# Optimization experiments

Measured on AMD Instinct MI355X. Metric: run time of the kernel, lower is better.

Reference implementation:

```python
import jax, jax.numpy as jnp
import numpy as np

D = 1024
H = 16
HD = D // H
FF = 4096
B, S = 2, 2048


def _ln(x, g, b, eps):
    mu = jnp.mean(x, axis=-1, keepdims=True)
    var = jnp.mean(jnp.square(x - mu), axis=-1, keepdims=True)
    return (x - mu) * jax.lax.rsqrt(var + eps) * g + b


def setup_inputs() -> dict:
    key = jax.random.key(0)
    ks = jax.random.split(key, 12)
    s = 0.02
    return {
        "x": jax.random.normal(ks[0], (B, S, D), jnp.float32),
        "attention_mask": jnp.ones((B, 1, 1, S), jnp.int32),
        "wq": jax.random.normal(ks[1], (D, D), jnp.float32) * s,
        "bq": jnp.zeros((D,), jnp.float32),
        "wk": jax.random.normal(ks[2], (D, D), jnp.float32) * s,
        "bk": jnp.zeros((D,), jnp.float32),
        "wv": jax.random.normal(ks[3], (D, D), jnp.float32) * s,
        "bv": jnp.zeros((D,), jnp.float32),
        "wo": jax.random.normal(ks[4], (D, D), jnp.float32) * s,
        "bo": jnp.zeros((D,), jnp.float32),
        "ln1_g": jnp.ones((D,), jnp.float32),
        "ln1_b": jnp.zeros((D,), jnp.float32),
        "w1": jax.random.normal(ks[5], (D, FF), jnp.float32) * s,
        "b1": jnp.zeros((FF,), jnp.float32),
        "w2": jax.random.normal(ks[6], (FF, D), jnp.float32) * s,
        "b2": jnp.zeros((D,), jnp.float32),
        "lnf_g": jnp.ones((D,), jnp.float32),
        "lnf_b": jnp.zeros((D,), jnp.float32),
        "ln2_g": jnp.ones((D,), jnp.float32),
        "ln2_b": jnp.zeros((D,), jnp.float32),
    }


def reference(x, attention_mask, wq, bq, wk, bk, wv, bv, wo, bo,
              ln1_g, ln1_b, w1, b1, w2, b2, lnf_g, lnf_b, ln2_g, ln2_b):
    b, s, d = x.shape
    # --- naive multi-head self-attention ---
    q = (x @ wq + bq).reshape(b, s, H, HD).transpose(0, 2, 1, 3)  # [b,h,s,hd]
    k = (x @ wk + bk).reshape(b, s, H, HD).transpose(0, 2, 1, 3)
    v = (x @ wv + bv).reshape(b, s, H, HD).transpose(0, 2, 1, 3)
    scores = jnp.einsum('bhqd,bhkd->bhqk', q, k) / jnp.sqrt(jnp.float32(HD))
    scores = jnp.where(attention_mask == 0, jnp.float32(-1e9), scores)
    attn = jax.nn.softmax(scores, axis=-1)
    ctx = jnp.einsum('bhqk,bhkd->bhqd', attn, v)
    ctx = ctx.transpose(0, 2, 1, 3).reshape(b, s, d)
    attn_out = ctx @ wo + bo
    # residual + LayerNorm (eps=1e-5, torch default)
    x1 = _ln(x + attn_out, ln1_g, ln1_b, 1e-5)
    # --- BERT-style FFN with internal residual LN (eps=1e-12) ---
    h = jax.nn.gelu(x1 @ w1 + b1, approximate=False)
    ff = _ln(h @ w2 + b2 + x1, lnf_g, lnf_b, 1e-12)
    # --- outer residual + LayerNorm (eps=1e-5) ---
    return _ln(x1 + ff, ln2_g, ln2_b, 1e-5)
```

## Files before the change

kernel.cpp:

```cpp
#include <hip/hip_runtime.h>

#define DMODEL 1024
#define NHEAD  16
#define HDIM   64
#define FFDIM  4096
#define BATCH  2
#define SEQ    2048
#define MTOK   (BATCH*SEQ)

typedef __bf16 bf16;
typedef __bf16 bf16x8 __attribute__((ext_vector_type(8)));
typedef float  floatx4 __attribute__((ext_vector_type(4)));
typedef unsigned int u32;

__device__ __forceinline__ int get_flag(const void* ln1g) {
  return (((const u32*)ln1g)[0] == 0x3F800000u) ? 0 : 1;
}
__device__ __forceinline__ float ld_ext(const void* p, size_t i, int flag) {
  return flag ? (float)((const bf16*)p)[i] : ((const float*)p)[i];
}

__device__ __forceinline__ void gload16(const bf16* g, bf16* lds_uniform) {
  __builtin_amdgcn_global_load_lds(
      (const __attribute__((address_space(1))) u32*)g,
      (__attribute__((address_space(3))) u32*)lds_uniform, 16, 0, 0);
}

__device__ __forceinline__ float gelu_f(float v) {
  float a = fabsf(v) * 0.70710678118654752f;
  float t = 1.0f / (1.0f + 0.3275911f * a);
  float poly = t * (0.254829592f + t * (-0.284496736f + t * (1.421413741f +
               t * (-1.453152027f + t * 1.061405429f))));
  float erf_abs = 1.0f - poly * __expf(-a * a);
  float erfv = copysignf(erf_abs, v);
  return 0.5f * v * (1.0f + erfv);
}

__global__ __launch_bounds__(256) void prep(
    const void* wq, const void* wk, const void* wv, const void* wo,
    const void* w1, const void* w2, const void* x,
    bf16* WTqkv, bf16* WToT, bf16* WT1, bf16* WT2, bf16* xC,
    const void* ln1g)
{
  int flag = get_flag(ln1g);
  int bid = blockIdx.x;
  if (bid >= 12288) {
    size_t base = (size_t)(bid - 12288) * 1024;
    int i = threadIdx.x * 4;
    #pragma unroll
    for (int j = 0; j < 4; j++) xC[base + i + j] = (bf16)ld_ext(x, base + i + j, flag);
    return;
  }
  __shared__ bf16 tile[32][33];
  const void* in; bf16* out; int K, N, t;
  if      (bid < 1024)  { in = wq; out = WTqkv;                 K = 1024; N = 1024; t = bid; }
  else if (bid < 2048)  { in = wk; out = WTqkv + 1024 * 1024;   K = 1024; N = 1024; t = bid - 1024; }
  else if (bid < 3072)  { in = wv; out = WTqkv + 2 * 1024 * 1024; K = 1024; N = 1024; t = bid - 2048; }
  else if (bid < 4096)  { in = wo; out = WToT;                  K = 1024; N = 1024; t = bid - 3072; }
  else if (bid < 8192)  { in = w1; out = WT1;                   K = 1024; N = 4096; t = bid - 4096; }
  else                  { in = w2; out = WT2;                   K = 4096; N = 1024; t = bid - 8192; }
  int shift = (N == 4096) ? 7 : 5;
  int k0 = (t >> shift) * 32, n0 = (t & ((1 << shift) - 1)) * 32;
  int tx = threadIdx.x & 31, ty = threadIdx.x >> 5;
  #pragma unroll
  for (int i = ty; i < 32; i += 8)
    tile[i][tx] = (bf16)ld_ext(in, (size_t)(k0 + i) * N + n0 + tx, flag);
  __syncthreads();
  #pragma unroll
  for (int i = ty; i < 32; i += 8)
    out[(size_t)(n0 + i) * K + k0 + tx] = tile[tx][i];
}

__global__ __launch_bounds__(256) void gemm128(
    const bf16* __restrict__ A, const bf16* __restrict__ BT,
    const void* __restrict__ bias0, const void* __restrict__ bias1,
    const void* __restrict__ bias2,
    bf16* __restrict__ out0, bf16* __restrict__ out1, bf16* __restrict__ out2,
    int N, int K, int ksub, int mode, const void* __restrict__ ln1g)
{
  __shared__ __align__(16) char smem[34816];
  bf16* As = (bf16*)smem;
  bf16* Bs = (bf16*)(smem + 16384);
  int flag = get_flag(ln1g);

  int tid = threadIdx.x, lane = tid & 63, w = tid >> 6;
  int wm = w & 1, wn = w >> 1;
  int m0 = blockIdx.x * 128, n0 = blockIdx.y * 128;
  int kstart = blockIdx.z * ksub;
  int r15 = lane & 15, kg = lane >> 4;

  floatx4 acc[4][4];
  #pragma unroll
  for (int mt = 0; mt < 4; mt++)
    #pragma unroll
    for (int nt = 0; nt < 4; nt++) acc[mt][nt] = (floatx4){0.f, 0.f, 0.f, 0.f};

  int srowA = (lane >> 3) & 7;
  int skc = (lane & 7) ^ srowA;

  for (int k0 = kstart; k0 < kstart + ksub; k0 += 64) {
    #pragma unroll
    for (int j = 0; j < 4; j++) {
      int c = w * 256 + j * 64 + lane;
      int row = c >> 3;
      gload16(A  + (size_t)(m0 + row) * K + k0 + skc * 8, As + (size_t)(w * 256 + j * 64) * 8);
      gload16(BT + (size_t)(n0 + row) * K + k0 + skc * 8, Bs + (size_t)(w * 256 + j * 64) * 8);
    }
    __syncthreads();

    #pragma unroll
    for (int kk = 0; kk < 2; kk++) {
      bf16x8 af[4], bfr[4];
      #pragma unroll
      for (int mt = 0; mt < 4; mt++) {
        int row = wm * 64 + mt * 16 + r15;
        int slot = (kk * 4 + kg) ^ (r15 & 7);
        af[mt] = *(const bf16x8*)&As[(row * 8 + slot) * 8];
      }
      #pragma unroll
      for (int nt = 0; nt < 4; nt++) {
        int row = wn * 64 + nt * 16 + r15;
        int slot = (kk * 4 + kg) ^ (r15 & 7);
        bfr[nt] = *(const bf16x8*)&Bs[(row * 8 + slot) * 8];
      }
      #pragma unroll
      for (int mt = 0; mt < 4; mt++)
        #pragma unroll
        for (int nt = 0; nt < 4; nt++)
          acc[mt][nt] = __builtin_amdgcn_mfma_f32_16x16x32_bf16(af[mt], bfr[nt], acc[mt][nt], 0, 0, 0);
    }
    __syncthreads();
  }

  bf16* scr = (bf16*)(smem + 8704 * w);
  int gcb = n0 + wn * 64;
  int which = (mode == 1) ? (gcb >> 10) : 0;
  int rowg0 = m0 + wm * 64;

  #pragma unroll
  for (int nt = 0; nt < 4; nt++) {
    int lcol = nt * 16 + r15;
    int gcol = gcb + lcol;
    int bidx = (mode == 1) ? (gcol & 1023) : gcol;
    const void* bp = (mode == 1) ? ((which == 0) ? bias0 : (which == 1) ? bias1 : bias2) : bias0;
    float bv = (blockIdx.z == 0) ? ld_ext(bp, bidx, flag) : 0.f;
    #pragma unroll
    for (int mt = 0; mt < 4; mt++) {
      #pragma unroll
      for (int r = 0; r < 4; r++) {
        int lrow = mt * 16 + kg * 4 + r;
        float val = acc[mt][nt][r] + bv;
        if (mode == 2) val = gelu_f(val);
        if (mode == 1 && which == 2) scr[lcol * 68 + lrow] = (bf16)val;
        else                         scr[lrow * 68 + lcol] = (bf16)val;
      }
    }
  }
  __syncthreads();

  bf16* outp = out0 + (size_t)blockIdx.z * MTOK * N;
  #pragma unroll
  for (int it = 0; it < 8; it++) {
    int c = it * 64 + lane;
    int rr = c >> 3, part = c & 7;
    bf16x8 vdat = *(const bf16x8*)&scr[rr * 68 + part * 8];
    bf16* dst;
    if (mode == 1) {
      if (which == 2) {
        int h = (gcb - 2048) >> 6, hd = rr;
        int b = rowg0 >> 11, s0 = rowg0 & 2047;
        dst = out2 + ((size_t)(b * NHEAD + h) * HDIM + hd) * SEQ + s0 + part * 8;
      } else {
        int rowg = rowg0 + rr;
        int b = rowg >> 11, s = rowg & 2047;
        int h = (gcb & 1023) >> 6;
        bf16* o = (which == 0) ? out0 : out1;
        dst = o + ((size_t)(b * NHEAD + h) * SEQ + s) * HDIM + part * 8;
      }
    } else {
      dst = outp + (size_t)(rowg0 + rr) * N + gcb + part * 8;
    }
    *(bf16x8*)dst = vdat;
  }
}

__global__ __launch_bounds__(256) void attn_mfma(
    const bf16* __restrict__ q, const bf16* __restrict__ k,
    const bf16* __restrict__ vt, const int* __restrict__ mask,
    bf16* __restrict__ ctx)
{
  __shared__ __align__(16) bf16 Ks[64][72];
  __shared__ __align__(16) bf16 Vts[64][72];
  __shared__ __align__(16) bf16 Ps[4][16][72];
  __shared__ float MaddS[64];

  int tid = threadIdx.x, lane = tid & 63, w = tid >> 6;
  int r15 = lane & 15, kg = lane >> 4;
  int bh = blockIdx.x >> 5;
  int qt = blockIdx.x & 31;
  int b = bh >> 4, h = bh & 15;
  int q0 = qt * 64 + w * 16;

  bf16x8 qf[2];
  #pragma unroll
  for (int kt2 = 0; kt2 < 2; kt2++)
    qf[kt2] = *(const bf16x8*)(q + ((size_t)bh * SEQ + q0 + r15) * HDIM + kt2 * 32 + kg * 8);

  bf16x8 ones;
  #pragma unroll
  for (int j = 0; j < 8; j++) ones[j] = (bf16)1.0f;

  floatx4 O[4];
  floatx4 lacc = (floatx4){0.f, 0.f, 0.f, 0.f};
  #pragma unroll
  for (int dt = 0; dt < 4; dt++) O[dt] = (floatx4){0.f, 0.f, 0.f, 0.f};

  for (int kt = 0; kt < SEQ; kt += 64) {
    #pragma unroll
    for (int j = 0; j < 2; j++) {
      int c = tid + j * 256;
      int row = c >> 3, cc = c & 7;
      *(bf16x8*)&Ks[row][cc * 8]  = *(const bf16x8*)(k  + ((size_t)bh * SEQ + kt + row) * HDIM + cc * 8);
      *(bf16x8*)&Vts[row][cc * 8] = *(const bf16x8*)(vt + ((size_t)bh * HDIM + row) * SEQ + kt + cc * 8);
    }
    if (tid < 64) MaddS[tid] = (mask[b * SEQ + kt + tid] == 0) ? -1e9f : 0.f;
    __syncthreads();

    floatx4 S[4];
    #pragma unroll
    for (int nt = 0; nt < 4; nt++) S[nt] = (floatx4){0.f, 0.f, 0.f, 0.f};
    #pragma unroll
    for (int nt = 0; nt < 4; nt++) {
      bf16x8 kf0 = *(const bf16x8*)&Ks[nt * 16 + r15][kg * 8];
      bf16x8 kf1 = *(const bf16x8*)&Ks[nt * 16 + r15][32 + kg * 8];
      S[nt] = __builtin_amdgcn_mfma_f32_16x16x32_bf16(qf[0], kf0, S[nt], 0, 0, 0);
      S[nt] = __builtin_amdgcn_mfma_f32_16x16x32_bf16(qf[1], kf1, S[nt], 0, 0, 0);
    }

    float madd[4];
    #pragma unroll
    for (int nt = 0; nt < 4; nt++) madd[nt] = MaddS[nt * 16 + r15];
    #pragma unroll
    for (int r = 0; r < 4; r++) {
      #pragma unroll
      for (int nt = 0; nt < 4; nt++) {
        float s = S[nt][r] * 0.125f + madd[nt];
        Ps[w][kg * 4 + r][nt * 16 + r15] = (bf16)__expf(fminf(s, 30.f));
      }
    }

    bf16x8 pa0 = *(const bf16x8*)&Ps[w][r15][kg * 8];
    bf16x8 pa1 = *(const bf16x8*)&Ps[w][r15][32 + kg * 8];
    #pragma unroll
    for (int dt = 0; dt < 4; dt++) {
      bf16x8 vf0 = *(const bf16x8*)&Vts[dt * 16 + r15][kg * 8];
      bf16x8 vf1 = *(const bf16x8*)&Vts[dt * 16 + r15][32 + kg * 8];
      O[dt] = __builtin_amdgcn_mfma_f32_16x16x32_bf16(pa0, vf0, O[dt], 0, 0, 0);
      O[dt] = __builtin_amdgcn_mfma_f32_16x16x32_bf16(pa1, vf1, O[dt], 0, 0, 0);
    }
    lacc = __builtin_amdgcn_mfma_f32_16x16x32_bf16(pa0, ones, lacc, 0, 0, 0);
    lacc = __builtin_amdgcn_mfma_f32_16x16x32_bf16(pa1, ones, lacc, 0, 0, 0);
    __syncthreads();
  }

  float inv[4];
  #pragma unroll
  for (int r = 0; r < 4; r++) inv[r] = 1.f / lacc[r];
  #pragma unroll
  for (int dt = 0; dt < 4; dt++)
    #pragma unroll
    for (int r = 0; r < 4; r++) {
      int srow = q0 + kg * 4 + r;
      int col = h * 64 + dt * 16 + r15;
      ctx[((size_t)b * SEQ + srow) * DMODEL + col] = (bf16)(O[dt][r] * inv[r]);
    }
}

__global__ __launch_bounds__(256) void ln_kernel(
    const bf16* ba, const bf16* bb, const bf16* bc,
    const void* g, const void* be,
    float eps, bf16* outb, void* out_ext, const void* ln1g)
{
  __shared__ float red1[4], red2[4];
  int flag = get_flag(ln1g);
  size_t base = (size_t)blockIdx.x * DMODEL;
  float v[4];
  #pragma unroll
  for (int i = 0; i < 4; i++) {
    int idx = threadIdx.x + i * 256;
    float s = (float)ba[base + idx];
    if (bb) s += (float)bb[base + idx];
    if (bc) s += (float)bc[base + idx];
    v[i] = s;
  }
  float sum = v[0] + v[1] + v[2] + v[3];
  #pragma unroll
  for (int o = 32; o > 0; o >>= 1) sum += __shfl_xor(sum, o);
  if ((threadIdx.x & 63) == 0) red1[threadIdx.x >> 6] = sum;
  __syncthreads();
  float mean = (red1[0] + red1[1] + red1[2] + red1[3]) * (1.f / DMODEL);
  float sq = 0.f;
  #pragma unroll
  for (int i = 0; i < 4; i++) { v[i] -= mean; sq += v[i] * v[i]; }
  #pragma unroll
  for (int o = 32; o > 0; o >>= 1) sq += __shfl_xor(sq, o);
  if ((threadIdx.x & 63) == 0) red2[threadIdx.x >> 6] = sq;
  __syncthreads();
  float rstd = rsqrtf((red2[0] + red2[1] + red2[2] + red2[3]) * (1.f / DMODEL) + eps);
  #pragma unroll
  for (int i = 0; i < 4; i++) {
    int idx = threadIdx.x + i * 256;
    float y = v[i] * rstd * ld_ext(g, idx, flag) + ld_ext(be, idx, flag);
    if (out_ext) {
      if (flag) ((bf16*)out_ext)[base + idx] = (bf16)y;
      else      ((float*)out_ext)[base + idx] = y;
    } else {
      outb[base + idx] = (bf16)y;
    }
  }
}

extern "C" void kernel_launch(void* const* d_in, const int* in_sizes, int n_in,
                              void* d_out, int out_size, void* d_ws, size_t ws_size,
                              hipStream_t stream) {
  const void* x    = d_in[0];
  const int*  msk  = (const int*)d_in[1];
  const void* wq   = d_in[2];
  const void* bq   = d_in[3];
  const void* wk   = d_in[4];
  const void* bk   = d_in[5];
  const void* wv   = d_in[6];
  const void* bv   = d_in[7];
  const void* wo   = d_in[8];
  const void* bo   = d_in[9];
  const void* ln1g = d_in[10];
  const void* ln1b = d_in[11];
  const void* w1   = d_in[12];
  const void* b1   = d_in[13];
  const void* w2   = d_in[14];
  const void* b2   = d_in[15];
  const void* lnfg = d_in[16];
  const void* lnfb = d_in[17];
  const void* ln2g = d_in[18];
  const void* ln2b = d_in[19];

  const size_t MB = 1024 * 1024;
  char* p = (char*)d_ws;
  bf16* xC     = (bf16*)(p + 0 * MB);
  bf16* qb     = (bf16*)(p + 8 * MB);
  bf16* kb     = (bf16*)(p + 16 * MB);
  bf16* vtb    = (bf16*)(p + 24 * MB);
  bf16* ctxb   = (bf16*)(p + 32 * MB);
  bf16* WTqkv  = (bf16*)(p + 40 * MB);
  bf16* WToT   = (bf16*)(p + 46 * MB);
  bf16* WT1    = (bf16*)(p + 48 * MB);
  bf16* WT2    = (bf16*)(p + 56 * MB);
  bf16* ao     = (bf16*)(p + 8 * MB);
  bf16* x1b    = xC;
  bf16* hb     = (bf16*)(p + 8 * MB);
  bf16* ffp    = (bf16*)(p + 40 * MB);
  bf16* ffb    = (bf16*)(p + 8 * MB);

  prep<<<16384, 256, 0, stream>>>(wq, wk, wv, wo, w1, w2, x,
                                  WTqkv, WToT, WT1, WT2, xC, ln1g);

  gemm128<<<dim3(MTOK / 128, 3072 / 128, 1), 256, 0, stream>>>(
      xC, WTqkv, bq, bk, bv, qb, kb, vtb, 3072, DMODEL, DMODEL, 1, ln1g);

  attn_mfma<<<BATCH * NHEAD * (SEQ / 64), 256, 0, stream>>>(qb, kb, vtb, msk, ctxb);

  gemm128<<<dim3(MTOK / 128, DMODEL / 128, 2), 256, 0, stream>>>(
      ctxb, WToT, bo, nullptr, nullptr, ao, nullptr, nullptr, DMODEL, DMODEL, 512, 3, ln1g);

  ln_kernel<<<MTOK, 256, 0, stream>>>(ao, ao + (size_t)MTOK * DMODEL, xC, ln1g, ln1b,
                                      1e-5f, x1b, nullptr, ln1g);

  gemm128<<<dim3(MTOK / 128, FFDIM / 128, 1), 256, 0, stream>>>(
      x1b, WT1, b1, nullptr, nullptr, hb, nullptr, nullptr, FFDIM, DMODEL, DMODEL, 2, ln1g);

  gemm128<<<dim3(MTOK / 128, DMODEL / 128, 2), 256, 0, stream>>>(
      hb, WT2, b2, nullptr, nullptr, ffp, nullptr, nullptr, DMODEL, FFDIM, 2048, 3, ln1g);

  ln_kernel<<<MTOK, 256, 0, stream>>>(ffp, ffp + (size_t)MTOK * DMODEL, x1b, lnfg, lnfb,
                                      1e-12f, ffb, nullptr, ln1g);

  ln_kernel<<<MTOK, 256, 0, stream>>>(x1b, ffb, nullptr, ln2g, ln2b, 1e-5f, nullptr, d_out, ln1g);
}
```

Baseline: 426.2 us.

## Fold softmax scale into Q and apply key mask through V and row-sum

```diff
diff --git a/kernel.cpp b/kernel.cpp
--- a/kernel.cpp
+++ b/kernel.cpp
@@ -10,8 +10,10 @@
 
 typedef __bf16 bf16;
 typedef __bf16 bf16x8 __attribute__((ext_vector_type(8)));
+typedef __bf16 bf16x4 __attribute__((ext_vector_type(4)));
 typedef float  floatx4 __attribute__((ext_vector_type(4)));
 typedef unsigned int u32;
+typedef unsigned int u32x4 __attribute__((ext_vector_type(4)));
 
 __device__ __forceinline__ int get_flag(const void* ln1g) {
   return (((const u32*)ln1g)[0] == 0x3F800000u) ? 0 : 1;
@@ -38,12 +40,27 @@
 
 __global__ __launch_bounds__(256) void prep(
     const void* wq, const void* wk, const void* wv, const void* wo,
-    const void* w1, const void* w2, const void* x,
+    const void* w1, const void* w2, const void* x, const int* mask,
     bf16* WTqkv, bf16* WToT, bf16* WT1, bf16* WT2, bf16* xC,
-    const void* ln1g)
+    u32* mwAll, bf16* m01All, const void* ln1g)
 {
   int flag = get_flag(ln1g);
   int bid = blockIdx.x;
+  if (bid >= 16384) {
+    int b = bid - 16384;
+    int base = b * SEQ + threadIdx.x * 8;
+    #pragma unroll
+    for (int j = 0; j < 8; j++)
+      m01All[base + j] = (bf16)(mask[base + j] ? 1.0f : 0.0f);
+    #pragma unroll
+    for (int t = 0; t < 4; t++) {
+      int k0 = threadIdx.x * 8 + 2 * t;
+      u32 mw = (mask[b * SEQ + k0] ? 0x0000FFFFu : 0u) |
+               (mask[b * SEQ + k0 + 1] ? 0xFFFF0000u : 0u);
+      mwAll[b * (SEQ / 2) + threadIdx.x * 4 + t] = mw;
+    }
+    return;
+  }
   if (bid >= 12288) {
     size_t base = (size_t)(bid - 12288) * 1024;
     int i = threadIdx.x * 4;
@@ -151,6 +168,7 @@
         int lrow = mt * 16 + kg * 4 + r;
         float val = acc[mt][nt][r] + bv;
         if (mode == 2) val = gelu_f(val);
+        if (mode == 1 && which == 0) val *= 0.125f;
         if (mode == 1 && which == 2) scr[lcol * 68 + lrow] = (bf16)val;
         else                         scr[lrow * 68 + lcol] = (bf16)val;
       }
@@ -186,13 +204,12 @@
 
 __global__ __launch_bounds__(256) void attn_mfma(
     const bf16* __restrict__ q, const bf16* __restrict__ k,
-    const bf16* __restrict__ vt, const int* __restrict__ mask,
-    bf16* __restrict__ ctx)
+    const bf16* __restrict__ vt, const u32* __restrict__ mwAll,
+    const bf16* __restrict__ m01All, bf16* __restrict__ ctx)
 {
-  __shared__ __align__(16) bf16 Ks[64][72];
-  __shared__ __align__(16) bf16 Vts[64][72];
-  __shared__ __align__(16) bf16 Ps[4][16][72];
-  __shared__ float MaddS[64];
+  __shared__ __align__(16) bf16 Ks[64][80];
+  __shared__ __align__(16) bf16 Vts[64][80];
+  __shared__ __align__(16) bf16 Ps[4][16][80];
 
   int tid = threadIdx.x, lane = tid & 63, w = tid >> 6;
   int r15 = lane & 15, kg = lane >> 4;
@@ -206,10 +223,6 @@
   for (int kt2 = 0; kt2 < 2; kt2++)
     qf[kt2] = *(const bf16x8*)(q + ((size_t)bh * SEQ + q0 + r15) * HDIM + kt2 * 32 + kg * 8);
 
-  bf16x8 ones;
-  #pragma unroll
-  for (int j = 0; j < 8; j++) ones[j] = (bf16)1.0f;
-
   floatx4 O[4];
   floatx4 lacc = (floatx4){0.f, 0.f, 0.f, 0.f};
   #pragma unroll
@@ -220,10 +233,12 @@
     for (int j = 0; j < 2; j++) {
       int c = tid + j * 256;
       int row = c >> 3, cc = c & 7;
-      *(bf16x8*)&Ks[row][cc * 8]  = *(const bf16x8*)(k  + ((size_t)bh * SEQ + kt + row) * HDIM + cc * 8);
-      *(bf16x8*)&Vts[row][cc * 8] = *(const bf16x8*)(vt + ((size_t)bh * HDIM + row) * SEQ + kt + cc * 8);
-    }
-    if (tid < 64) MaddS[tid] = (mask[b * SEQ + kt + tid] == 0) ? -1e9f : 0.f;
+      *(bf16x8*)&Ks[row][cc * 8] = *(const bf16x8*)(k + ((size_t)bh * SEQ + kt + row) * HDIM + cc * 8);
+      u32x4 vv = *(const u32x4*)(vt + ((size_t)bh * HDIM + row) * SEQ + kt + cc * 8);
+      u32x4 mw = *(const u32x4*)&mwAll[(size_t)b * (SEQ / 2) + (kt + cc * 8) / 2];
+      vv &= mw;
+      *(u32x4*)&Vts[row][cc * 8] = vv;
+    }
     __syncthreads();
 
     floatx4 S[4];
@@ -233,24 +248,22 @@
     for (int nt = 0; nt < 4; nt++) {
       bf16x8 kf0 = *(const bf16x8*)&Ks[nt * 16 + r15][kg * 8];
       bf16x8 kf1 = *(const bf16x8*)&Ks[nt * 16 + r15][32 + kg * 8];
-      S[nt] = __builtin_amdgcn_mfma_f32_16x16x32_bf16(qf[0], kf0, S[nt], 0, 0, 0);
-      S[nt] = __builtin_amdgcn_mfma_f32_16x16x32_bf16(qf[1], kf1, S[nt], 0, 0, 0);
-    }
-
-    float madd[4];
-    #pragma unroll
-    for (int nt = 0; nt < 4; nt++) madd[nt] = MaddS[nt * 16 + r15];
-    #pragma unroll
-    for (int r = 0; r < 4; r++) {
+      S[nt] = __builtin_amdgcn_mfma_f32_16x16x32_bf16(kf0, qf[0], S[nt], 0, 0, 0);
+      S[nt] = __builtin_amdgcn_mfma_f32_16x16x32_bf16(kf1, qf[1], S[nt], 0, 0, 0);
+    }
+
+    #pragma unroll
+    for (int nt = 0; nt < 4; nt++) {
+      bf16x4 pk;
       #pragma unroll
-      for (int nt = 0; nt < 4; nt++) {
-        float s = S[nt][r] * 0.125f + madd[nt];
-        Ps[w][kg * 4 + r][nt * 16 + r15] = (bf16)__expf(fminf(s, 30.f));
-      }
+      for (int r = 0; r < 4; r++) pk[r] = (bf16)__expf(S[nt][r]);
+      *(bf16x4*)&Ps[w][r15][nt * 16 + kg * 4] = pk;
     }
 
     bf16x8 pa0 = *(const bf16x8*)&Ps[w][r15][kg * 8];
     bf16x8 pa1 = *(const bf16x8*)&Ps[w][r15][32 + kg * 8];
+    bf16x8 m01f0 = *(const bf16x8*)&m01All[(size_t)b * SEQ + kt + kg * 8];
+    bf16x8 m01f1 = *(const bf16x8*)&m01All[(size_t)b * SEQ + kt + 32 + kg * 8];
     #pragma unroll
     for (int dt = 0; dt < 4; dt++) {
       bf16x8 vf0 = *(const bf16x8*)&Vts[dt * 16 + r15][kg * 8];
@@ -258,8 +271,8 @@
       O[dt] = __builtin_amdgcn_mfma_f32_16x16x32_bf16(pa0, vf0, O[dt], 0, 0, 0);
       O[dt] = __builtin_amdgcn_mfma_f32_16x16x32_bf16(pa1, vf1, O[dt], 0, 0, 0);
     }
-    lacc = __builtin_amdgcn_mfma_f32_16x16x32_bf16(pa0, ones, lacc, 0, 0, 0);
-    lacc = __builtin_amdgcn_mfma_f32_16x16x32_bf16(pa1, ones, lacc, 0, 0, 0);
+    lacc = __builtin_amdgcn_mfma_f32_16x16x32_bf16(pa0, m01f0, lacc, 0, 0, 0);
+    lacc = __builtin_amdgcn_mfma_f32_16x16x32_bf16(pa1, m01f1, lacc, 0, 0, 0);
     __syncthreads();
   }
 
@@ -360,14 +373,16 @@
   bf16* hb     = (bf16*)(p + 8 * MB);
   bf16* ffp    = (bf16*)(p + 40 * MB);
   bf16* ffb    = (bf16*)(p + 8 * MB);
-
-  prep<<<16384, 256, 0, stream>>>(wq, wk, wv, wo, w1, w2, x,
-                                  WTqkv, WToT, WT1, WT2, xC, ln1g);
+  u32*  mwAll  = (u32*)d_out;
+  bf16* m01All = (bf16*)((char*)d_out + 8192);
+
+  prep<<<16386, 256, 0, stream>>>(wq, wk, wv, wo, w1, w2, x, msk,
+                                  WTqkv, WToT, WT1, WT2, xC, mwAll, m01All, ln1g);
 
   gemm128<<<dim3(MTOK / 128, 3072 / 128, 1), 256, 0, stream>>>(
       xC, WTqkv, bq, bk, bv, qb, kb, vtb, 3072, DMODEL, DMODEL, 1, ln1g);
 
-  attn_mfma<<<BATCH * NHEAD * (SEQ / 64), 256, 0, stream>>>(qb, kb, vtb, msk, ctxb);
+  attn_mfma<<<BATCH * NHEAD * (SEQ / 64), 256, 0, stream>>>(qb, kb, vtb, mwAll, m01All, ctxb);
 
   gemm128<<<dim3(MTOK / 128, DMODEL / 128, 2), 256, 0, stream>>>(
       ctxb, WToT, bo, nullptr, nullptr, ao, nullptr, nullptr, DMODEL, DMODEL, 512, 3, ln1g);
```

Result: faster. 409.2 us (-4.0%).
